# Kernel optimization log

Measured on AMD Instinct MI355X. Metric: run time of the kernel, lower is better.

## Reference

```python
import jax, jax.numpy as jnp
import numpy as np

B, V, M, C = 1024, 2, 256, 256  # batch, num_vars (must be 2), latent states, categories


def setup_inputs() -> dict:
    key = jax.random.key(0)
    k1, k2, k3 = jax.random.split(key, 3)
    x = jax.random.randint(k1, (B, V), 0, C)
    # input-node tables: per var v, per latent node k, a [M, C] row-normalized table
    W = jax.nn.softmax(jax.random.normal(k2, (V, M, M, C), dtype=jnp.float32), axis=-1)
    # sum-node mixture weights over the M product children
    w_sum = jax.nn.softmax(jax.random.normal(k3, (M,), dtype=jnp.float32))
    return {"x": x, "W": W, "w_sum": w_sum}


def reference(x, W, w_sum):
    # lp[v] has shape [M(k), M(m), B]: log W[v, k, m, x[b, v]]
    # (matches torch: probs[:, x_var].log() per input node, stacked over latent k)
    lp0 = jnp.log(W[0][:, :, x[:, 0]])  # [M, M, B]
    lp1 = jnp.log(W[1][:, :, x[:, 1]])  # [M, M, B]
    prod = lp0 + lp1                    # product nodes, [M(k), M, B]
    # sum node: log( sum_k w_k * exp(prod_k) ) -> [M, B]
    mixed = jnp.log(jnp.einsum('k,kmb->mb', w_sum, jnp.exp(prod)))
    # root: logsumexp over the leading M dim -> [B]
    return jax.nn.logsumexp(mixed, axis=0)
```

## Files before the change

### kernel.cpp

```cpp
#include <hip/hip_runtime.h>
#include <math.h>


#define SPLITS  128
#define KCHUNK  512
#define BK      32
#define NITER   (KCHUNK / BK)
#define LDSS    40

typedef float  f32x4  __attribute__((ext_vector_type(4)));
typedef short  bf16x8 __attribute__((ext_vector_type(8)));

static __device__ __forceinline__ short f2bf(float f) {
    unsigned u = __builtin_bit_cast(unsigned, f);
    u += 0x7fffu + ((u >> 16) & 1u);
    return (short)(u >> 16);
}

template <bool USE_PART>
__global__ __launch_bounds__(512, 2) void gemm_s_kernel(
    const float* __restrict__ W, const float* __restrict__ wsum,
    float* __restrict__ out_acc)
{
    __shared__ short As[256 * LDSS];
    __shared__ short Bs[128 * LDSS];

    const int  c1tile = blockIdx.x;
    const int  split  = blockIdx.y;
    const long kbase  = (long)split * KCHUNK;

    const float* __restrict__ Ag = W;
    const float* __restrict__ Bg = W + 16777216 + (long)c1tile * 128;

    const int t = threadIdx.x;
    const int cqA = (t & 63) * 4;
    const int kqA = (t >> 6) * 4;
    const int cqB = (t & 31) * 4;
    const int kqB = (t >> 5) * 2;

    const int lane = t & 63;
    const int wv   = t >> 6;
    const int wc0  = (wv & 3) * 64;
    const int wc1  = (wv >> 2) * 64;
    const int ml   = lane & 15;
    const int qd   = lane >> 4;

    const float w0 = wsum[split * 2];
    const float w1 = wsum[split * 2 + 1];

    f32x4 acc[4][4];
#pragma unroll
    for (int i = 0; i < 4; ++i)
#pragma unroll
        for (int j = 0; j < 4; ++j) acc[i][j] = (f32x4){0.f, 0.f, 0.f, 0.f};

    for (int it = 0; it < NITER; ++it) {
        const long  k0 = kbase + (long)it * BK;
        const float wk = (it < NITER / 2) ? w0 : w1;
        float4 a4[4], b4[2];
#pragma unroll
        for (int r = 0; r < 4; ++r)
            a4[r] = *(const float4*)(Ag + (k0 + kqA + r) * 256 + cqA);
#pragma unroll
        for (int r = 0; r < 2; ++r)
            b4[r] = *(const float4*)(Bg + (k0 + kqB + r) * 256 + cqB);
        __syncthreads();
        const float* af32 = reinterpret_cast<const float*>(a4);
        const float* bf32 = reinterpret_cast<const float*>(b4);
#pragma unroll
        for (int j = 0; j < 4; ++j) {
            short4 av;
            av.x = f2bf(af32[0 * 4 + j] * wk);
            av.y = f2bf(af32[1 * 4 + j] * wk);
            av.z = f2bf(af32[2 * 4 + j] * wk);
            av.w = f2bf(af32[3 * 4 + j] * wk);
            *(short4*)&As[(cqA + j) * LDSS + kqA] = av;
            short2 bv;
            bv.x = f2bf(bf32[0 * 4 + j]);
            bv.y = f2bf(bf32[1 * 4 + j]);
            *(short2*)&Bs[(cqB + j) * LDSS + kqB] = bv;
        }
        __syncthreads();
        bf16x8 afr[4];
#pragma unroll
        for (int mi = 0; mi < 4; ++mi)
            afr[mi] = *(const bf16x8*)&As[(wc0 + mi * 16 + ml) * LDSS + qd * 8];
#pragma unroll
        for (int ni = 0; ni < 4; ++ni) {
            const bf16x8 bfr = *(const bf16x8*)&Bs[(wc1 + ni * 16 + ml) * LDSS + qd * 8];
#pragma unroll
            for (int mi = 0; mi < 4; ++mi)
                acc[mi][ni] = __builtin_amdgcn_mfma_f32_16x16x32_bf16(
                    afr[mi], bfr, acc[mi][ni], 0, 0, 0);
        }
    }

    if (USE_PART) {
        float* __restrict__ Pb = out_acc + ((size_t)split * 2 + c1tile) * 32768;
#pragma unroll
        for (int mi = 0; mi < 4; ++mi) {
            const int row0 = wc0 + mi * 16 + qd * 4;
#pragma unroll
            for (int ni = 0; ni < 4; ++ni) {
                const int col = wc1 + ni * 16 + ml;
#pragma unroll
                for (int r = 0; r < 4; ++r)
                    Pb[(row0 + r) * 128 + col] = acc[mi][ni][r];
            }
        }
    } else {
#pragma unroll
        for (int mi = 0; mi < 4; ++mi) {
            const int row0 = wc0 + mi * 16 + qd * 4;
#pragma unroll
            for (int ni = 0; ni < 4; ++ni) {
                const int col = c1tile * 128 + wc1 + ni * 16 + ml;
#pragma unroll
                for (int r = 0; r < 4; ++r)
                    atomicAdd(&out_acc[(row0 + r) * 256 + col], acc[mi][ni][r]);
            }
        }
    }
}

__global__ __launch_bounds__(64) void finish_part_kernel(
    const int* __restrict__ x, const float* __restrict__ P, float* __restrict__ out)
{
    const int b  = blockIdx.x;
    const int t  = threadIdx.x;
    const int x0 = x[2 * b], x1 = x[2 * b + 1];
    const int t1 = x1 >> 7;
    const size_t base = (size_t)x0 * 128 + (x1 & 127);
    float v = P[((size_t)t * 2 + t1) * 32768 + base]
            + P[((size_t)(t + 64) * 2 + t1) * 32768 + base];
#pragma unroll
    for (int off = 32; off > 0; off >>= 1) v += __shfl_down(v, off);
    if (t == 0) out[b] = logf(v);
}

__global__ __launch_bounds__(64) void finish_atom_kernel(
    const int* __restrict__ x, const float* __restrict__ S, float* __restrict__ out)
{
    const int b  = blockIdx.x * 64 + threadIdx.x;
    const int x0 = x[2 * b], x1 = x[2 * b + 1];
    out[b] = logf(S[x0 * 256 + x1]);
}

extern "C" void kernel_launch(void* const* d_in, const int* in_sizes, int n_in,
                              void* d_out, int out_size, void* d_ws, size_t ws_size,
                              hipStream_t stream)
{
    const int*   x    = (const int*)d_in[0];
    const float* W    = (const float*)d_in[1];
    const float* wsum = (const float*)d_in[2];
    float* out = (float*)d_out;

    const size_t part_bytes = (size_t)SPLITS * 2 * 32768 * sizeof(float);

    if (ws_size >= part_bytes) {
        float* P = (float*)d_ws;
        gemm_s_kernel<true><<<dim3(2, SPLITS), 512, 0, stream>>>(W, wsum, P);
        finish_part_kernel<<<dim3(1024), 64, 0, stream>>>(x, P, out);
    } else {
        float* S = (float*)d_ws;
        hipMemsetAsync(d_ws, 0, 65536 * sizeof(float), stream);
        gemm_s_kernel<false><<<dim3(2, SPLITS), 512, 0, stream>>>(W, wsum, S);
        finish_atom_kernel<<<dim3(16), 64, 0, stream>>>(x, S, out);
    }
}
```

Before: 208.9 us.

## Use full 256x256 tiles per split with double-buffered LDS prefetch

Each block now computes the full 256x256 output tile for one k-split (one latent k per block), so the A operand is no longer reloaded by two column tiles. The main loop is software-pipelined: global loads for the next chunk are issued before the MFMA work on the current LDS buffer, with two LDS buffers and a single barrier per iteration. The cost is a larger accumulator footprint (128 floats per thread) and double LDS, which may reduce occupancy. The partial-sum workspace also doubles in size, so the finish kernel reads four partials per lane.

```diff
diff --git a/kernel.cpp b/kernel.cpp
--- a/kernel.cpp
+++ b/kernel.cpp
@@ -2,8 +2,8 @@
 #include <math.h>
 
 
-#define SPLITS  128
-#define KCHUNK  512
+#define SPLITS  256
+#define KCHUNK  256
 #define BK      32
 #define NITER   (KCHUNK / BK)
 #define LDSS    40
@@ -22,90 +22,114 @@
     const float* __restrict__ W, const float* __restrict__ wsum,
     float* __restrict__ out_acc)
 {
-    __shared__ short As[256 * LDSS];
-    __shared__ short Bs[128 * LDSS];
+    __shared__ short As[2][256 * LDSS];
+    __shared__ short Bs[2][256 * LDSS];
 
-    const int  c1tile = blockIdx.x;
-    const int  split  = blockIdx.y;
-    const long kbase  = (long)split * KCHUNK;
+    const int  split = blockIdx.x;
+    const long kbase = (long)split * KCHUNK;
+    const float wk   = wsum[split];
 
-    const float* __restrict__ Ag = W;
-    const float* __restrict__ Bg = W + 16777216 + (long)c1tile * 128;
+    const float* __restrict__ Ag = W + kbase * 256;
+    const float* __restrict__ Bg = W + 16777216 + kbase * 256;
 
-    const int t = threadIdx.x;
-    const int cqA = (t & 63) * 4;
-    const int kqA = (t >> 6) * 4;
-    const int cqB = (t & 31) * 4;
-    const int kqB = (t >> 5) * 2;
+    const int t  = threadIdx.x;
+    const int cq = (t & 63) * 4;
+    const int kq = (t >> 6) * 4;
 
     const int lane = t & 63;
     const int wv   = t >> 6;
     const int wc0  = (wv & 3) * 64;
-    const int wc1  = (wv >> 2) * 64;
+    const int wc1  = (wv >> 2) * 128;
     const int ml   = lane & 15;
     const int qd   = lane >> 4;
 
-    const float w0 = wsum[split * 2];
-    const float w1 = wsum[split * 2 + 1];
-
-    f32x4 acc[4][4];
+    f32x4 acc[4][8];
 #pragma unroll
     for (int i = 0; i < 4; ++i)
 #pragma unroll
-        for (int j = 0; j < 4; ++j) acc[i][j] = (f32x4){0.f, 0.f, 0.f, 0.f};
+        for (int j = 0; j < 8; ++j) acc[i][j] = (f32x4){0.f, 0.f, 0.f, 0.f};
 
-    for (int it = 0; it < NITER; ++it) {
-        const long  k0 = kbase + (long)it * BK;
-        const float wk = (it < NITER / 2) ? w0 : w1;
-        float4 a4[4], b4[2];
+    float4 a4[4], b4[4];
+
 #pragma unroll
-        for (int r = 0; r < 4; ++r)
-            a4[r] = *(const float4*)(Ag + (k0 + kqA + r) * 256 + cqA);
-#pragma unroll
-        for (int r = 0; r < 2; ++r)
-            b4[r] = *(const float4*)(Bg + (k0 + kqB + r) * 256 + cqB);
-        __syncthreads();
+    for (int r = 0; r < 4; ++r) {
+        a4[r] = *(const float4*)(Ag + (long)(kq + r) * 256 + cq);
+        b4[r] = *(const float4*)(Bg + (long)(kq + r) * 256 + cq);
+    }
+    {
         const float* af32 = reinterpret_cast<const float*>(a4);
         const float* bf32 = reinterpret_cast<const float*>(b4);
 #pragma unroll
         for (int j = 0; j < 4; ++j) {
-            short4 av;
+            short4 av, bv;
             av.x = f2bf(af32[0 * 4 + j] * wk);
             av.y = f2bf(af32[1 * 4 + j] * wk);
             av.z = f2bf(af32[2 * 4 + j] * wk);
             av.w = f2bf(af32[3 * 4 + j] * wk);
-            *(short4*)&As[(cqA + j) * LDSS + kqA] = av;
-            short2 bv;
             bv.x = f2bf(bf32[0 * 4 + j]);
             bv.y = f2bf(bf32[1 * 4 + j]);
-            *(short2*)&Bs[(cqB + j) * LDSS + kqB] = bv;
+            bv.z = f2bf(bf32[2 * 4 + j]);
+            bv.w = f2bf(bf32[3 * 4 + j]);
+            *(short4*)&As[0][(cq + j) * LDSS + kq] = av;
+            *(short4*)&Bs[0][(cq + j) * LDSS + kq] = bv;
         }
-        __syncthreads();
+    }
+    __syncthreads();
+
+#pragma unroll
+    for (int it = 0; it < NITER; ++it) {
+        const int cur = it & 1;
+        if (it + 1 < NITER) {
+#pragma unroll
+            for (int r = 0; r < 4; ++r) {
+                a4[r] = *(const float4*)(Ag + (long)((it + 1) * BK + kq + r) * 256 + cq);
+                b4[r] = *(const float4*)(Bg + (long)((it + 1) * BK + kq + r) * 256 + cq);
+            }
+        }
         bf16x8 afr[4];
 #pragma unroll
         for (int mi = 0; mi < 4; ++mi)
-            afr[mi] = *(const bf16x8*)&As[(wc0 + mi * 16 + ml) * LDSS + qd * 8];
+            afr[mi] = *(const bf16x8*)&As[cur][(wc0 + mi * 16 + ml) * LDSS + qd * 8];
 #pragma unroll
-        for (int ni = 0; ni < 4; ++ni) {
-            const bf16x8 bfr = *(const bf16x8*)&Bs[(wc1 + ni * 16 + ml) * LDSS + qd * 8];
+        for (int ni = 0; ni < 8; ++ni) {
+            const bf16x8 bfr = *(const bf16x8*)&Bs[cur][(wc1 + ni * 16 + ml) * LDSS + qd * 8];
 #pragma unroll
             for (int mi = 0; mi < 4; ++mi)
                 acc[mi][ni] = __builtin_amdgcn_mfma_f32_16x16x32_bf16(
                     afr[mi], bfr, acc[mi][ni], 0, 0, 0);
         }
+        if (it + 1 < NITER) {
+            const float* af32 = reinterpret_cast<const float*>(a4);
+            const float* bf32 = reinterpret_cast<const float*>(b4);
+#pragma unroll
+            for (int j = 0; j < 4; ++j) {
+                short4 av, bv;
+                av.x = f2bf(af32[0 * 4 + j] * wk);
+                av.y = f2bf(af32[1 * 4 + j] * wk);
+                av.z = f2bf(af32[2 * 4 + j] * wk);
+                av.w = f2bf(af32[3 * 4 + j] * wk);
+                bv.x = f2bf(bf32[0 * 4 + j]);
+                bv.y = f2bf(bf32[1 * 4 + j]);
+                bv.z = f2bf(bf32[2 * 4 + j]);
+                bv.w = f2bf(bf32[3 * 4 + j]);
+                *(short4*)&As[1 - cur][(cq + j) * LDSS + kq] = av;
+                *(short4*)&Bs[1 - cur][(cq + j) * LDSS + kq] = bv;
+            }
+            __syncthreads();
+        }
     }
 
     if (USE_PART) {
-        float* __restrict__ Pb = out_acc + ((size_t)split * 2 + c1tile) * 32768;
+        float* __restrict__ Pb = out_acc + (size_t)split * 65536;
 #pragma unroll
         for (int mi = 0; mi < 4; ++mi) {
             const int row0 = wc0 + mi * 16 + qd * 4;
 #pragma unroll
-            for (int ni = 0; ni < 4; ++ni) {
+            for (int ni = 0; ni < 8; ++ni) {
                 const int col = wc1 + ni * 16 + ml;
 #pragma unroll
                 for (int r = 0; r < 4; ++r)
-                    Pb[(row0 + r) * 128 + col] = acc[mi][ni][r];
+                    Pb[(row0 + r) * 256 + col] = acc[mi][ni][r];
             }
         }
     } else {
@@ -113,8 +137,8 @@
         for (int mi = 0; mi < 4; ++mi) {
             const int row0 = wc0 + mi * 16 + qd * 4;
 #pragma unroll
-            for (int ni = 0; ni < 4; ++ni) {
-                const int col = c1tile * 128 + wc1 + ni * 16 + ml;
+            for (int ni = 0; ni < 8; ++ni) {
+                const int col = wc1 + ni * 16 + ml;
 #pragma unroll
                 for (int r = 0; r < 4; ++r)
                     atomicAdd(&out_acc[(row0 + r) * 256 + col], acc[mi][ni][r]);
@@ -129,10 +153,11 @@
     const int b  = blockIdx.x;
     const int t  = threadIdx.x;
     const int x0 = x[2 * b], x1 = x[2 * b + 1];
-    const int t1 = x1 >> 7;
-    const size_t base = (size_t)x0 * 128 + (x1 & 127);
-    float v = P[((size_t)t * 2 + t1) * 32768 + base]
-            + P[((size_t)(t + 64) * 2 + t1) * 32768 + base];
+    const size_t base = (size_t)x0 * 256 + x1;
+    float v = 0.f;
+#pragma unroll
+    for (int j = 0; j < 4; ++j)
+        v += P[(size_t)(t + 64 * j) * 65536 + base];
 #pragma unroll
     for (int off = 32; off > 0; off >>= 1) v += __shfl_down(v, off);
     if (t == 0) out[b] = logf(v);
@@ -155,16 +180,16 @@
     const float* wsum = (const float*)d_in[2];
     float* out = (float*)d_out;
 
-    const size_t part_bytes = (size_t)SPLITS * 2 * 32768 * sizeof(float);
+    const size_t part_bytes = (size_t)SPLITS * 65536 * sizeof(float);
 
     if (ws_size >= part_bytes) {
         float* P = (float*)d_ws;
-        gemm_s_kernel<true><<<dim3(2, SPLITS), 512, 0, stream>>>(W, wsum, P);
+        gemm_s_kernel<true><<<dim3(SPLITS), 512, 0, stream>>>(W, wsum, P);
         finish_part_kernel<<<dim3(1024), 64, 0, stream>>>(x, P, out);
     } else {
         float* S = (float*)d_ws;
         hipMemsetAsync(d_ws, 0, 65536 * sizeof(float), stream);
-        gemm_s_kernel<false><<<dim3(2, SPLITS), 512, 0, stream>>>(W, wsum, S);
+        gemm_s_kernel<false><<<dim3(SPLITS), 512, 0, stream>>>(W, wsum, S);
         finish_atom_kernel<<<dim3(16), 64, 0, stream>>>(x, S, out);
     }
 }
```

New measurement: 211.5 us. About the same (+1.2%).
